# Kernel tuning notes

Hardware: AMD Instinct MI355X
Metric: run time of the kernel (lower is better)

Reference implementation:

```python
import jax, jax.numpy as jnp
import numpy as np

N, S, C, K, V = 8, 8192, 1, 1024, 64  # batch, samples, n_channels, n_classes, vec_len


def setup_inputs() -> dict:
    key = jax.random.key(0)
    k1, k2 = jax.random.split(key)
    x0 = jax.random.normal(k1, (N, S, C, V), dtype=jnp.float32)
    embedding0 = jax.random.normal(k2, (C, K, V), dtype=jnp.float32) * 0.001
    return {"x0": x0, "embedding0": embedding0}


def reference(x0, embedding0):
    # normalize=False path of the original module
    x = x0
    emb = embedding0
    Ns = x.shape[0] * x.shape[1]
    xf = x.reshape(Ns, C, V)  # (Ns, C, V)
    # squared distances ||x - e||^2 without materializing (Ns, C, K, V)
    d2 = (
        jnp.sum(xf * xf, axis=-1)[:, :, None]
        - 2.0 * jnp.einsum("ncv,ckv->nck", xf, emb)
        + jnp.sum(emb * emb, axis=-1)[None, :, :]
    )
    index = jnp.argmin(d2, axis=2)  # (Ns, C); argmin of dist == argmin of dist^2
    # histogram entropy (matches torch histc over bins 0..K-1, divided by len(index)=Ns)
    counts = jnp.zeros((K,), jnp.float32).at[index.reshape(-1)].add(1.0)
    prob = counts / Ns
    safe_log = jnp.log(jnp.where(counts > 0, prob, 1.0))
    entropy = -jnp.sum(jnp.where(counts > 0, prob * safe_log, 0.0))
    # gather codewords: embedding[c, index[n,c]]
    output = emb[jnp.arange(C)[None, :], index].reshape(x.shape)
    out0 = jax.lax.stop_gradient(output - x) + x  # straight-through
    out1 = jnp.sum((jax.lax.stop_gradient(x) - output) ** 2, axis=-1)  # (N,S,C)
    out2 = jnp.sum((x - jax.lax.stop_gradient(output)) ** 2, axis=-1)  # (N,S,C)
    return (out0, out1, out2, entropy)
```

## Files before the change

### kernel.cpp

```cpp
#include <hip/hip_runtime.h>
#include <math.h>

#define NS   65536
#define KK   1024
#define VV   64
#define SPB  128
#define NB   (NS / SPB)
#define CHC  256
#define NCHK (KK / CHC)
#define TPC  (CHC / 16)
#define CHB  (CHC * VV * 2)

#define OUT0_OFF 0
#define OUT1_OFF 4194304
#define OUT2_OFF 4259840
#define ENT_OFF  4325376


typedef __attribute__((ext_vector_type(8))) short bf16x8;
typedef __attribute__((ext_vector_type(4))) float f32x4;

#define ASYNC16(gp, lp) __builtin_amdgcn_global_load_lds(                      \
    (const __attribute__((address_space(1))) unsigned int*)(gp),               \
    (__attribute__((address_space(3))) unsigned int*)(lp), 16, 0, 0)

__device__ __forceinline__ short f2bf(float f) {
    unsigned u = __float_as_uint(f);
    u = (u + 0x7fffu + ((u >> 16) & 1u)) >> 16;
    return (short)u;
}

__global__ void vq_prep(const float* __restrict__ emb, unsigned int* __restrict__ hist,
                        float* __restrict__ cinit, short* __restrict__ cb,
                        unsigned int* __restrict__ entCnt) {
    int t = blockIdx.x * blockDim.x + threadIdx.x;
    if (t == 0) entCnt[0] = 0u;
    if (t < KK) {
        hist[t] = 0u;
        const float4* e4 = (const float4*)(emb + (size_t)t * VV);
        const int ch = t >> 8, cw = t & 255;
        short* base = cb + (size_t)ch * (CHC * VV) + cw * 64;
        float s = 0.f;
        union { short sh[8]; bf16x8 v; } pk;
        #pragma unroll
        for (int g = 0; g < 8; ++g) {
            float4 f0 = e4[2 * g], f1 = e4[2 * g + 1];
            s = fmaf(f0.x, f0.x, s); s = fmaf(f0.y, f0.y, s);
            s = fmaf(f0.z, f0.z, s); s = fmaf(f0.w, f0.w, s);
            s = fmaf(f1.x, f1.x, s); s = fmaf(f1.y, f1.y, s);
            s = fmaf(f1.z, f1.z, s); s = fmaf(f1.w, f1.w, s);
            pk.sh[0] = f2bf(f0.x); pk.sh[1] = f2bf(f0.y);
            pk.sh[2] = f2bf(f0.z); pk.sh[3] = f2bf(f0.w);
            pk.sh[4] = f2bf(f1.x); pk.sh[5] = f2bf(f1.y);
            pk.sh[6] = f2bf(f1.z); pk.sh[7] = f2bf(f1.w);
            *(bf16x8*)(base + ((g ^ (cw & 7)) * 8)) = pk.v;
        }
        cinit[t] = 1.0f - 0.5f * s;
    }
}

__global__ __launch_bounds__(256, 2) void vq_main(
    const float* __restrict__ x, const float* __restrict__ emb,
    const float* __restrict__ cinit, const short* __restrict__ cb,
    unsigned int* __restrict__ hist,
    float* __restrict__ out0, float* __restrict__ out1, float* __restrict__ out2,
    float* __restrict__ entOut)
{
    __shared__ __align__(16) char  sCB[2][CHB];
    __shared__ __align__(16) float sCI[KK];
    __shared__ unsigned sPk[SPB];
    __shared__ float    sXn[SPB];
    __shared__ float    sPart[4];
    __shared__ unsigned sLast;

    const int tid  = threadIdx.x;
    const int lane = tid & 63;
    const int wv   = tid >> 6;
    const int col  = lane & 15;
    const int quad = lane >> 4;
    const int samp0 = blockIdx.x * SPB;
    const int wbase = wv * 32;

    {
        const char* g0 = (const char*)cb;
        #pragma unroll
        for (int i = 0; i < 8; ++i) {
            const int off = (i * 256 + tid) * 16;
            ASYNC16(g0 + off, sCB[0] + off);
        }
        ((float4*)sCI)[tid] = ((const float4*)cinit)[tid];
    }

    bf16x8 a[4];
    float  xn[2];
    #pragma unroll
    for (int mt = 0; mt < 2; ++mt) {
        const float* xp = x + (size_t)(samp0 + wbase + mt * 16 + col) * VV + quad * 8;
        float4 p0 = *(const float4*)(xp);
        float4 p1 = *(const float4*)(xp + 4);
        float4 p2 = *(const float4*)(xp + 32);
        float4 p3 = *(const float4*)(xp + 36);
        bf16x8 lo, hi;
        lo[0]=f2bf(p0.x); lo[1]=f2bf(p0.y); lo[2]=f2bf(p0.z); lo[3]=f2bf(p0.w);
        lo[4]=f2bf(p1.x); lo[5]=f2bf(p1.y); lo[6]=f2bf(p1.z); lo[7]=f2bf(p1.w);
        hi[0]=f2bf(p2.x); hi[1]=f2bf(p2.y); hi[2]=f2bf(p2.z); hi[3]=f2bf(p2.w);
        hi[4]=f2bf(p3.x); hi[5]=f2bf(p3.y); hi[6]=f2bf(p3.z); hi[7]=f2bf(p3.w);
        a[2 * mt] = lo; a[2 * mt + 1] = hi;
        float s = 0.f;
        s=fmaf(p0.x,p0.x,s); s=fmaf(p0.y,p0.y,s); s=fmaf(p0.z,p0.z,s); s=fmaf(p0.w,p0.w,s);
        s=fmaf(p1.x,p1.x,s); s=fmaf(p1.y,p1.y,s); s=fmaf(p1.z,p1.z,s); s=fmaf(p1.w,p1.w,s);
        s=fmaf(p2.x,p2.x,s); s=fmaf(p2.y,p2.y,s); s=fmaf(p2.z,p2.z,s); s=fmaf(p2.w,p2.w,s);
        s=fmaf(p3.x,p3.x,s); s=fmaf(p3.y,p3.y,s); s=fmaf(p3.z,p3.z,s); s=fmaf(p3.w,p3.w,s);
        xn[mt] = s;
    }
    #pragma unroll
    for (int mt = 0; mt < 2; ++mt) {
        xn[mt] += __shfl_xor(xn[mt], 16, 64);
        xn[mt] += __shfl_xor(xn[mt], 32, 64);
    }
    __syncthreads();

    unsigned pm[8];
    #pragma unroll
    for (int j = 0; j < 8; ++j) pm[j] = 0u;

    const int rb0off = col * 128 + ((quad ^ (col & 7)) << 4);
    const int rb1off = col * 128 + (((4 + quad) ^ (col & 7)) << 4);
    const unsigned invc = 1023u - (unsigned)col;

    for (int ch = 0; ch < NCHK; ++ch) {
        if (ch + 1 < NCHK) {
            const char* g = (const char*)cb + (size_t)(ch + 1) * CHB;
            char* nb = sCB[(ch + 1) & 1];
            #pragma unroll
            for (int i = 0; i < 8; ++i) {
                const int off = (i * 256 + tid) * 16;
                ASYNC16(g + off, nb + off);
            }
        }
        const char* B = sCB[ch & 1];
        const unsigned invch = invc - (unsigned)(ch * CHC);
        unsigned pkp[8];
        #pragma unroll
        for (int tl = 0; tl < TPC; ++tl) {
            bf16x8 b0 = *(const bf16x8*)(B + tl * 2048 + rb0off);
            bf16x8 b1 = *(const bf16x8*)(B + tl * 2048 + rb1off);
            float ci = sCI[ch * CHC + tl * 16 + col];
            f32x4 cv = {ci, ci, ci, ci};
            const unsigned inv = invch - (unsigned)(tl * 16);
            unsigned pk2[8];
            #pragma unroll
            for (int mt = 0; mt < 2; ++mt) {
                f32x4 acc = __builtin_amdgcn_mfma_f32_16x16x32_bf16(a[2*mt],     b0, cv,  0, 0, 0);
                acc       = __builtin_amdgcn_mfma_f32_16x16x32_bf16(a[2*mt + 1], b1, acc, 0, 0, 0);
                #pragma unroll
                for (int r = 0; r < 4; ++r)
                    pk2[mt*4+r] = (__float_as_uint(acc[r]) & 0xFFFFFC00u) | inv;
            }
            if (tl & 1) {
                #pragma unroll
                for (int j = 0; j < 8; ++j) {
                    unsigned t2 = pkp[j] > pk2[j] ? pkp[j] : pk2[j];
                    pm[j] = pm[j] > t2 ? pm[j] : t2;
                }
            } else {
                #pragma unroll
                for (int j = 0; j < 8; ++j) pkp[j] = pk2[j];
            }
        }
        __syncthreads();
    }

    #pragma unroll
    for (int off = 1; off < 16; off <<= 1) {
        #pragma unroll
        for (int j = 0; j < 8; ++j) {
            unsigned o = (unsigned)__shfl_xor((int)pm[j], off, 64);
            pm[j] = (o > pm[j]) ? o : pm[j];
        }
    }
    if (col == 0) {
        #pragma unroll
        for (int mt = 0; mt < 2; ++mt)
            #pragma unroll
            for (int r = 0; r < 4; ++r)
                sPk[wbase + mt * 16 + quad * 4 + r] = pm[mt * 4 + r];
    }
    if (quad == 0) {
        #pragma unroll
        for (int mt = 0; mt < 2; ++mt) sXn[wbase + mt * 16 + col] = xn[mt];
    }
    __syncthreads();

    if (tid < SPB) {
        unsigned p = sPk[tid];
        int   code = 1023 - (int)(p & 1023u);
        float sf   = __uint_as_float(p & 0xFFFFFC00u);
        float d    = fmaf(-2.f, sf - 1.0f, sXn[tid]);
        int n = samp0 + tid;
        out1[n] = d;
        out2[n] = d;
        atomicAdd(&hist[code], 1u);
    }
    {
        const int smp  = tid >> 1;
        const int half = tid & 1;
        const int code = 1023 - (int)(sPk[smp] & 1023u);
        const float4* src = (const float4*)(emb + (size_t)code * VV + half * 32);
        float4*       dst = (float4*)(out0 + (size_t)(samp0 + smp) * VV + half * 32);
        #pragma unroll
        for (int i = 0; i < 8; ++i) dst[i] = src[i];
    }

    __syncthreads();
    unsigned int* entCnt = (unsigned int*)entOut;
    if (tid == 0) sLast = (atomicAdd(entCnt, 1u) == (NB - 1)) ? 1u : 0u;
    __syncthreads();
    if (sLast) {
        float e = 0.f;
        #pragma unroll
        for (int i = 0; i < 4; ++i) {
            unsigned c = atomicAdd(&hist[i * 256 + tid], 0u);
            if (c) { float p = (float)c * (1.0f / (float)NS); e -= p * logf(p); }
        }
        #pragma unroll
        for (int off = 32; off > 0; off >>= 1) e += __shfl_down(e, off, 64);
        if (lane == 0) sPart[wv] = e;
        __syncthreads();
        if (tid == 0) entOut[0] = sPart[0] + sPart[1] + sPart[2] + sPart[3];
    }
}

extern "C" void kernel_launch(void* const* d_in, const int* in_sizes, int n_in,
                              void* d_out, int out_size, void* d_ws, size_t ws_size,
                              hipStream_t stream) {
    const float* x   = (const float*)d_in[0];
    const float* emb = (const float*)d_in[1];
    float* out = (float*)d_out;
    unsigned int* hist  = (unsigned int*)d_ws;
    float*        cinit = (float*)((char*)d_ws + 4096);
    short*        cb    = (short*)((char*)d_ws + 8192);

    vq_prep<<<4, 256, 0, stream>>>(emb, hist, cinit, cb, (unsigned int*)(out + ENT_OFF));
    vq_main<<<NB, 256, 0, stream>>>(x, emb, cinit, cb, hist,
                                    out + OUT0_OFF, out + OUT1_OFF, out + OUT2_OFF,
                                    out + ENT_OFF);
}
```

Baseline: 102.5 us.

## Load full codebook into LDS once and split K across wave groups

Replaces the double-buffered 256-codeword chunk loop with a single 128KB LDS load of the whole bf16 codebook. Blocks grow to 1024 threads handling 256 samples, and two wave groups each scan half of the codewords; their packed argmin results are merged in shared memory. This removes the per-chunk barriers and halves the number of blocks, so each codebook load is amortised over twice as many samples. The cost is 128KB+ of LDS per block, which limits occupancy to roughly one block per CU, and a serialized initial load with no overlap. The gather into out0 and the final entropy reduction are also reorganised for the larger block.

```diff
diff --git a/kernel.cpp b/kernel.cpp
--- a/kernel.cpp
+++ b/kernel.cpp
@@ -4,12 +4,9 @@
 #define NS   65536
 #define KK   1024
 #define VV   64
-#define SPB  128
+#define SPB  256
 #define NB   (NS / SPB)
-#define CHC  256
-#define NCHK (KK / CHC)
-#define TPC  (CHC / 16)
-#define CHB  (CHC * VV * 2)
+#define CBB  131072
 
 #define OUT0_OFF 0
 #define OUT1_OFF 4194304
@@ -39,7 +36,7 @@
         hist[t] = 0u;
         const float4* e4 = (const float4*)(emb + (size_t)t * VV);
         const int ch = t >> 8, cw = t & 255;
-        short* base = cb + (size_t)ch * (CHC * VV) + cw * 64;
+        short* base = cb + (size_t)ch * (256 * VV) + cw * 64;
         float s = 0.f;
         union { short sh[8]; bf16x8 v; } pk;
         #pragma unroll
@@ -59,36 +56,38 @@
     }
 }
 
-__global__ __launch_bounds__(256, 2) void vq_main(
+__global__ __launch_bounds__(1024, 4) void vq_main(
     const float* __restrict__ x, const float* __restrict__ emb,
     const float* __restrict__ cinit, const short* __restrict__ cb,
     unsigned int* __restrict__ hist,
     float* __restrict__ out0, float* __restrict__ out1, float* __restrict__ out2,
     float* __restrict__ entOut)
 {
-    __shared__ __align__(16) char  sCB[2][CHB];
+    __shared__ __align__(16) char  sCB[CBB];
     __shared__ __align__(16) float sCI[KK];
-    __shared__ unsigned sPk[SPB];
+    __shared__ unsigned sPk2[2][SPB];
     __shared__ float    sXn[SPB];
-    __shared__ float    sPart[4];
+    __shared__ float    sPart[16];
     __shared__ unsigned sLast;
 
     const int tid  = threadIdx.x;
     const int lane = tid & 63;
     const int wv   = tid >> 6;
+    const int grp  = wv & 7;
+    const int kh   = wv >> 3;
     const int col  = lane & 15;
     const int quad = lane >> 4;
     const int samp0 = blockIdx.x * SPB;
-    const int wbase = wv * 32;
+    const int wbase = grp * 32;
 
     {
         const char* g0 = (const char*)cb;
         #pragma unroll
         for (int i = 0; i < 8; ++i) {
-            const int off = (i * 256 + tid) * 16;
-            ASYNC16(g0 + off, sCB[0] + off);
-        }
-        ((float4*)sCI)[tid] = ((const float4*)cinit)[tid];
+            const int off = (i * 1024 + tid) * 16;
+            ASYNC16(g0 + off, sCB + off);
+        }
+        sCI[tid] = cinit[tid];
     }
 
     bf16x8 a[4];
@@ -113,10 +112,12 @@
         s=fmaf(p3.x,p3.x,s); s=fmaf(p3.y,p3.y,s); s=fmaf(p3.z,p3.z,s); s=fmaf(p3.w,p3.w,s);
         xn[mt] = s;
     }
-    #pragma unroll
-    for (int mt = 0; mt < 2; ++mt) {
-        xn[mt] += __shfl_xor(xn[mt], 16, 64);
-        xn[mt] += __shfl_xor(xn[mt], 32, 64);
+    if (kh == 0) {
+        #pragma unroll
+        for (int mt = 0; mt < 2; ++mt) {
+            xn[mt] += __shfl_xor(xn[mt], 16, 64);
+            xn[mt] += __shfl_xor(xn[mt], 32, 64);
+        }
     }
     __syncthreads();
 
@@ -126,49 +127,37 @@
 
     const int rb0off = col * 128 + ((quad ^ (col & 7)) << 4);
     const int rb1off = col * 128 + (((4 + quad) ^ (col & 7)) << 4);
-    const unsigned invc = 1023u - (unsigned)col;
-
-    for (int ch = 0; ch < NCHK; ++ch) {
-        if (ch + 1 < NCHK) {
-            const char* g = (const char*)cb + (size_t)(ch + 1) * CHB;
-            char* nb = sCB[(ch + 1) & 1];
-            #pragma unroll
-            for (int i = 0; i < 8; ++i) {
-                const int off = (i * 256 + tid) * 16;
-                ASYNC16(g + off, nb + off);
+    const unsigned invc = 1023u - (unsigned)(kh * 512) - (unsigned)col;
+    const char*  B  = sCB + kh * 65536;
+    const float* CI = sCI + kh * 512;
+
+    unsigned pkp[8];
+    #pragma unroll 8
+    for (int t = 0; t < 32; ++t) {
+        bf16x8 b0 = *(const bf16x8*)(B + t * 2048 + rb0off);
+        bf16x8 b1 = *(const bf16x8*)(B + t * 2048 + rb1off);
+        float ci = CI[t * 16 + col];
+        f32x4 cv = {ci, ci, ci, ci};
+        const unsigned inv = invc - (unsigned)(t * 16);
+        unsigned pk2[8];
+        #pragma unroll
+        for (int mt = 0; mt < 2; ++mt) {
+            f32x4 acc = __builtin_amdgcn_mfma_f32_16x16x32_bf16(a[2*mt],     b0, cv,  0, 0, 0);
+            acc       = __builtin_amdgcn_mfma_f32_16x16x32_bf16(a[2*mt + 1], b1, acc, 0, 0, 0);
+            #pragma unroll
+            for (int r = 0; r < 4; ++r)
+                pk2[mt*4+r] = (__float_as_uint(acc[r]) & 0xFFFFFC00u) | inv;
+        }
+        if (t & 1) {
+            #pragma unroll
+            for (int j = 0; j < 8; ++j) {
+                unsigned t2 = pkp[j] > pk2[j] ? pkp[j] : pk2[j];
+                pm[j] = pm[j] > t2 ? pm[j] : t2;
             }
-        }
-        const char* B = sCB[ch & 1];
-        const unsigned invch = invc - (unsigned)(ch * CHC);
-        unsigned pkp[8];
-        #pragma unroll
-        for (int tl = 0; tl < TPC; ++tl) {
-            bf16x8 b0 = *(const bf16x8*)(B + tl * 2048 + rb0off);
-            bf16x8 b1 = *(const bf16x8*)(B + tl * 2048 + rb1off);
-            float ci = sCI[ch * CHC + tl * 16 + col];
-            f32x4 cv = {ci, ci, ci, ci};
-            const unsigned inv = invch - (unsigned)(tl * 16);
-            unsigned pk2[8];
-            #pragma unroll
-            for (int mt = 0; mt < 2; ++mt) {
-                f32x4 acc = __builtin_amdgcn_mfma_f32_16x16x32_bf16(a[2*mt],     b0, cv,  0, 0, 0);
-                acc       = __builtin_amdgcn_mfma_f32_16x16x32_bf16(a[2*mt + 1], b1, acc, 0, 0, 0);
-                #pragma unroll
-                for (int r = 0; r < 4; ++r)
-                    pk2[mt*4+r] = (__float_as_uint(acc[r]) & 0xFFFFFC00u) | inv;
-            }
-            if (tl & 1) {
-                #pragma unroll
-                for (int j = 0; j < 8; ++j) {
-                    unsigned t2 = pkp[j] > pk2[j] ? pkp[j] : pk2[j];
-                    pm[j] = pm[j] > t2 ? pm[j] : t2;
-                }
-            } else {
-                #pragma unroll
-                for (int j = 0; j < 8; ++j) pkp[j] = pk2[j];
-            }
-        }
-        __syncthreads();
+        } else {
+            #pragma unroll
+            for (int j = 0; j < 8; ++j) pkp[j] = pk2[j];
+        }
     }
 
     #pragma unroll
@@ -184,16 +173,18 @@
         for (int mt = 0; mt < 2; ++mt)
             #pragma unroll
             for (int r = 0; r < 4; ++r)
-                sPk[wbase + mt * 16 + quad * 4 + r] = pm[mt * 4 + r];
-    }
-    if (quad == 0) {
+                sPk2[kh][wbase + mt * 16 + quad * 4 + r] = pm[mt * 4 + r];
+    }
+    if (kh == 0 && quad == 0) {
         #pragma unroll
         for (int mt = 0; mt < 2; ++mt) sXn[wbase + mt * 16 + col] = xn[mt];
     }
     __syncthreads();
 
     if (tid < SPB) {
-        unsigned p = sPk[tid];
+        unsigned pa = sPk2[0][tid], pb = sPk2[1][tid];
+        unsigned p  = pa > pb ? pa : pb;
+        sPk2[0][tid] = p;
         int   code = 1023 - (int)(p & 1023u);
         float sf   = __uint_as_float(p & 0xFFFFFC00u);
         float d    = fmaf(-2.f, sf - 1.0f, sXn[tid]);
@@ -202,32 +193,41 @@
         out2[n] = d;
         atomicAdd(&hist[code], 1u);
     }
+    __syncthreads();
+
     {
-        const int smp  = tid >> 1;
-        const int half = tid & 1;
-        const int code = 1023 - (int)(sPk[smp] & 1023u);
-        const float4* src = (const float4*)(emb + (size_t)code * VV + half * 32);
-        float4*       dst = (float4*)(out0 + (size_t)(samp0 + smp) * VV + half * 32);
-        #pragma unroll
-        for (int i = 0; i < 8; ++i) dst[i] = src[i];
+        float4* dstB = (float4*)(out0 + (size_t)samp0 * VV);
+        #pragma unroll
+        for (int i = 0; i < 4; ++i) {
+            const int idx  = i * 1024 + tid;
+            const int smp  = idx >> 4;
+            const int part = idx & 15;
+            const int code = 1023 - (int)(sPk2[0][smp] & 1023u);
+            dstB[idx] = *((const float4*)(emb + (size_t)code * VV) + part);
+        }
     }
 
     __syncthreads();
     unsigned int* entCnt = (unsigned int*)entOut;
-    if (tid == 0) sLast = (atomicAdd(entCnt, 1u) == (NB - 1)) ? 1u : 0u;
+    if (tid == 0)
+        sLast = (__hip_atomic_fetch_add(entCnt, 1u, __ATOMIC_ACQ_REL,
+                                        __HIP_MEMORY_SCOPE_AGENT) == (NB - 1)) ? 1u : 0u;
     __syncthreads();
     if (sLast) {
+        unsigned c = __hip_atomic_load(&hist[tid], __ATOMIC_RELAXED,
+                                       __HIP_MEMORY_SCOPE_AGENT);
         float e = 0.f;
-        #pragma unroll
-        for (int i = 0; i < 4; ++i) {
-            unsigned c = atomicAdd(&hist[i * 256 + tid], 0u);
-            if (c) { float p = (float)c * (1.0f / (float)NS); e -= p * logf(p); }
-        }
+        if (c) { float p = (float)c * (1.0f / (float)NS); e = -p * logf(p); }
         #pragma unroll
         for (int off = 32; off > 0; off >>= 1) e += __shfl_down(e, off, 64);
         if (lane == 0) sPart[wv] = e;
         __syncthreads();
-        if (tid == 0) entOut[0] = sPart[0] + sPart[1] + sPart[2] + sPart[3];
+        if (tid == 0) {
+            float s = 0.f;
+            #pragma unroll
+            for (int i = 0; i < 16; ++i) s += sPart[i];
+            entOut[0] = s;
+        }
     }
 }
 
@@ -242,7 +242,7 @@
     short*        cb    = (short*)((char*)d_ws + 8192);
 
     vq_prep<<<4, 256, 0, stream>>>(emb, hist, cinit, cb, (unsigned int*)(out + ENT_OFF));
-    vq_main<<<NB, 256, 0, stream>>>(x, emb, cinit, cb, hist,
-                                    out + OUT0_OFF, out + OUT1_OFF, out + OUT2_OFF,
-                                    out + ENT_OFF);
-}
+    vq_main<<<NB, 1024, 0, stream>>>(x, emb, cinit, cb, hist,
+                                     out + OUT0_OFF, out + OUT1_OFF, out + OUT2_OFF,
+                                     out + ENT_OFF);
+}
```

Result: slower. 111.3 us (+8.6%).
